# Performance work log

Hardware: AMD Instinct MI355X
Metric: run time of the kernel (lower is better)

## Reference

```python
import jax, jax.numpy as jnp
import numpy as np

L, H, D, BINS = 4, 8, 512, 16
HD = D // H
DFF = 4 * D
EPS = 1e-5


def _ln(x, g, b):
    mu = jnp.mean(x, axis=-1, keepdims=True)
    var = jnp.var(x, axis=-1, keepdims=True)
    return (x - mu) * jax.lax.rsqrt(var + EPS) * g + b


def setup_inputs() -> dict:
    key = jax.random.key(0)
    ks = jax.random.split(key, 24)
    B, N, F = 8, 1024, 4
    s = 0.02
    inp = {
        'slot_features': jax.random.normal(ks[0], (B, N, F), jnp.float32),
        'distance_matrix': jax.random.uniform(ks[1], (B, N, N), jnp.float32),
        'slot_mask': jnp.ones((B, N), dtype=bool),
        # input projection (Linear 4->D, then ReLU, then LayerNorm)
        'in_w': jax.random.normal(ks[2], (F, D), jnp.float32) * s,
        'in_b': jnp.zeros((D,), jnp.float32),
        'in_g': jnp.ones((D,), jnp.float32),
        'in_beta': jnp.zeros((D,), jnp.float32),
        # learnable distance bias, init linspace(0,-2) per head
        'dist_bias': jnp.tile(jnp.linspace(0.0, -2.0, BINS, dtype=jnp.float32)[None, :], (H, 1)),
        # per-layer stacked params (weights stored [in,out])
        'qkv_w': jax.random.normal(ks[3], (L, D, 3 * D), jnp.float32) * s,
        'qkv_b': jnp.zeros((L, 3 * D), jnp.float32),
        'out_w': jax.random.normal(ks[4], (L, D, D), jnp.float32) * s,
        'out_b': jnp.zeros((L, D), jnp.float32),
        'ffn_w1': jax.random.normal(ks[5], (L, D, DFF), jnp.float32) * s,
        'ffn_b1': jnp.zeros((L, DFF), jnp.float32),
        'ffn_w2': jax.random.normal(ks[6], (L, DFF, D), jnp.float32) * s,
        'ffn_b2': jnp.zeros((L, D), jnp.float32),
        'n1_g': jnp.ones((L, D), jnp.float32),
        'n1_b': jnp.zeros((L, D), jnp.float32),
        'n2_g': jnp.ones((L, D), jnp.float32),
        'n2_b': jnp.zeros((L, D), jnp.float32),
        'op_w': jax.random.normal(ks[7], (D, D), jnp.float32) * s,
        'op_b': jnp.zeros((D,), jnp.float32),
    }
    return inp


def _distance_bias(distance_matrix, slot_mask, dist_bias):
    # (B,H,N,N) additive attention bias from binned normalized distances
    max_dist = jnp.clip(jnp.max(distance_matrix, axis=(-1, -2), keepdims=True), 1e-6, None)
    norm_dist = distance_matrix / max_dist
    bin_idx = jnp.clip((norm_dist * (BINS - 1)).astype(jnp.int32), 0, BINS - 1)  # (B,N,N)
    bias = jnp.transpose(dist_bias.T[bin_idx], (0, 3, 1, 2))  # (B,N,N,H)->(B,H,N,N)
    pad = ~(slot_mask[:, :, None] & slot_mask[:, None, :])  # (B,N,N)
    return jnp.where(pad[:, None, :, :], -jnp.inf, bias)


def reference(slot_features, distance_matrix, slot_mask, in_w, in_b, in_g, in_beta,
              dist_bias, qkv_w, qkv_b, out_w, out_b, ffn_w1, ffn_b1, ffn_w2, ffn_b2,
              n1_g, n1_b, n2_g, n2_b, op_w, op_b):
    B, N, _ = slot_features.shape
    h = _ln(jax.nn.relu(slot_features @ in_w + in_b), in_g, in_beta)  # (B,N,D)
    attn_bias = _distance_bias(distance_matrix, slot_mask, dist_bias)  # (B,H,N,N)
    scale = 1.0 / jnp.sqrt(jnp.float32(HD))
    for i in range(L):
        hn = _ln(h, n1_g[i], n1_b[i])
        qkv = (hn @ qkv_w[i] + qkv_b[i]).reshape(B, N, 3, H, HD)
        q, k, v = (jnp.transpose(qkv[:, :, j], (0, 2, 1, 3)) for j in range(3))  # (B,H,N,HD)
        scores = jnp.einsum('bhnd,bhmd->bhnm', q, k) * scale + attn_bias
        attn = jax.nn.softmax(scores, axis=-1)
        o = jnp.einsum('bhnm,bhmd->bhnd', attn, v)
        o = jnp.transpose(o, (0, 2, 1, 3)).reshape(B, N, D)
        h = h + (o @ out_w[i] + out_b[i])
        hn2 = _ln(h, n2_g[i], n2_b[i])
        ff = jax.nn.gelu(hn2 @ ffn_w1[i] + ffn_b1[i], approximate=False) @ ffn_w2[i] + ffn_b2[i]
        h = h + ff
    return h @ op_w + op_b
```

## Files before the change

kernel.cpp:

```cpp
#include <hip/hip_runtime.h>


typedef __attribute__((ext_vector_type(8))) short short8;
typedef __attribute__((ext_vector_type(4))) float f32x4;

__device__ __forceinline__ float b2f(unsigned short u){
  return __uint_as_float(((unsigned)u) << 16);
}
__device__ __forceinline__ unsigned short f2b(float f){
  unsigned u = __float_as_uint(f);
  u += 0x7fffU + ((u >> 16) & 1U);
  return (unsigned short)(u >> 16);
}
__device__ __forceinline__ void gload16(const void* g, void* l){
  __builtin_amdgcn_global_load_lds((const __attribute__((address_space(1))) void*)g,
                                   (__attribute__((address_space(3))) void*)l, 16, 0, 0);
}

__global__ void transpose_w(const float* __restrict__ src, unsigned short* __restrict__ dst,
                            int K, int N){
  __shared__ float tile[32][33];
  const float* s = src + (size_t)blockIdx.z * K * N;
  unsigned short* d = dst + (size_t)blockIdx.z * K * N;
  int j = threadIdx.x & 31, i0 = threadIdx.x >> 5;
  int kt = blockIdx.y * 32, nt = blockIdx.x * 32;
#pragma unroll
  for (int s4 = 0; s4 < 4; ++s4){
    int i = i0 + s4 * 8;
    tile[i][j] = s[(size_t)(kt + i) * N + nt + j];
  }
  __syncthreads();
#pragma unroll
  for (int s4 = 0; s4 < 4; ++s4){
    int i = i0 + s4 * 8;
    d[(size_t)(nt + i) * K + kt + j] = f2b(tile[j][i]);
  }
}

__global__ void vt_kernel(const unsigned short* __restrict__ qkv, unsigned short* __restrict__ vt){
  __shared__ unsigned short tile[32][33];
  int tt = blockIdx.x, dt = blockIdx.y, bh = blockIdx.z;
  int b = bh >> 3, h = bh & 7;
  int j = threadIdx.x & 31, i0 = threadIdx.x >> 5;
#pragma unroll
  for (int s4 = 0; s4 < 4; ++s4){
    int i = i0 + s4 * 8;
    tile[i][j] = qkv[(size_t)(b * 1024 + tt * 32 + i) * 1536 + 1024 + h * 64 + dt * 32 + j];
  }
  __syncthreads();
#pragma unroll
  for (int s4 = 0; s4 < 4; ++s4){
    int i = i0 + s4 * 8;
    vt[(size_t)(bh * 64 + dt * 32 + i) * 1024 + tt * 32 + j] = tile[j][i];
  }
}

__global__ void bmax_kernel(const float* __restrict__ dist, unsigned* __restrict__ bmax){
  int b = blockIdx.x >> 5, sl = blockIdx.x & 31;
  const float* p = dist + (size_t)b * 1048576 + sl * 32768;
  int t = threadIdx.x;
  float m = 0.f;
  for (int i = t * 4; i < 32768; i += 1024){
    float4 v = *(const float4*)(p + i);
    m = fmaxf(m, fmaxf(fmaxf(v.x, v.y), fmaxf(v.z, v.w)));
  }
#pragma unroll
  for (int o = 1; o < 64; o <<= 1) m = fmaxf(m, __shfl_xor(m, o));
  __shared__ float wm[4];
  if ((t & 63) == 0) wm[t >> 6] = m;
  __syncthreads();
  if (t == 0){
    m = fmaxf(fmaxf(wm[0], wm[1]), fmaxf(wm[2], wm[3]));
    atomicMax(bmax + b, __float_as_uint(m));
  }
}

__global__ void bins_kernel(const float* __restrict__ dist, const unsigned* __restrict__ bmax,
                            unsigned char* __restrict__ out){
  int flat = blockIdx.x * 256 + threadIdx.x;
  int l15 = flat & 15, kt = (flat >> 4) & 15, q = (flat >> 8) & 1023, b = flat >> 18;
  float mx = fmaxf(__uint_as_float(bmax[b]), 1e-6f);
  const float* p = dist + ((size_t)(b * 1024 + q)) * 1024 + kt * 64 + l15;
  unsigned wd = 0;
#pragma unroll
  for (int ks = 0; ks < 4; ++ks){
    float v = p[ks * 16];
    int bi = (int)((v / mx) * 15.0f); bi = bi < 0 ? 0 : (bi > 15 ? 15 : bi);
    wd |= (unsigned)bi << (ks * 8);
  }
  *(unsigned*)(out + ((size_t)(b * 1024 + q)) * 1024 + kt * 64 + l15 * 4) = wd;
}

__global__ void inproj_kernel(const float* __restrict__ x, const float* __restrict__ w,
                              const float* __restrict__ b, const float* __restrict__ g,
                              const float* __restrict__ be, float* __restrict__ h){
  int t = threadIdx.x, wv = t >> 6, lane = t & 63;
  int row = blockIdx.x * 4 + wv;
  float x0 = x[row * 4 + 0], x1 = x[row * 4 + 1], x2 = x[row * 4 + 2], x3 = x[row * 4 + 3];
  int c0 = lane * 4, c1 = 256 + lane * 4;
  float4 v0, v1; float s = 0.f, sq = 0.f;
  {
    float4 w0 = *(const float4*)(w + c0), w1 = *(const float4*)(w + 512 + c0);
    float4 w2 = *(const float4*)(w + 1024 + c0), w3 = *(const float4*)(w + 1536 + c0);
    float4 bb = *(const float4*)(b + c0);
    v0.x = fmaxf(0.f, x0*w0.x + x1*w1.x + x2*w2.x + x3*w3.x + bb.x);
    v0.y = fmaxf(0.f, x0*w0.y + x1*w1.y + x2*w2.y + x3*w3.y + bb.y);
    v0.z = fmaxf(0.f, x0*w0.z + x1*w1.z + x2*w2.z + x3*w3.z + bb.z);
    v0.w = fmaxf(0.f, x0*w0.w + x1*w1.w + x2*w2.w + x3*w3.w + bb.w);
    s += v0.x + v0.y + v0.z + v0.w;
    sq += v0.x*v0.x + v0.y*v0.y + v0.z*v0.z + v0.w*v0.w;
  }
  {
    float4 w0 = *(const float4*)(w + c1), w1 = *(const float4*)(w + 512 + c1);
    float4 w2 = *(const float4*)(w + 1024 + c1), w3 = *(const float4*)(w + 1536 + c1);
    float4 bb = *(const float4*)(b + c1);
    v1.x = fmaxf(0.f, x0*w0.x + x1*w1.x + x2*w2.x + x3*w3.x + bb.x);
    v1.y = fmaxf(0.f, x0*w0.y + x1*w1.y + x2*w2.y + x3*w3.y + bb.y);
    v1.z = fmaxf(0.f, x0*w0.z + x1*w1.z + x2*w2.z + x3*w3.z + bb.z);
    v1.w = fmaxf(0.f, x0*w0.w + x1*w1.w + x2*w2.w + x3*w3.w + bb.w);
    s += v1.x + v1.y + v1.z + v1.w;
    sq += v1.x*v1.x + v1.y*v1.y + v1.z*v1.z + v1.w*v1.w;
  }
#pragma unroll
  for (int o = 1; o < 64; o <<= 1){ s += __shfl_xor(s, o); sq += __shfl_xor(sq, o); }
  float mu = s * (1.f / 512.f);
  float var = sq * (1.f / 512.f) - mu * mu;
  float rs = rsqrtf(var + 1e-5f);
  float* hp = h + (size_t)row * 512;
  {
    float4 gg = *(const float4*)(g + c0), bb = *(const float4*)(be + c0);
    float4 o4;
    o4.x = (v0.x - mu) * rs * gg.x + bb.x; o4.y = (v0.y - mu) * rs * gg.y + bb.y;
    o4.z = (v0.z - mu) * rs * gg.z + bb.z; o4.w = (v0.w - mu) * rs * gg.w + bb.w;
    *(float4*)(hp + c0) = o4;
  }
  {
    float4 gg = *(const float4*)(g + c1), bb = *(const float4*)(be + c1);
    float4 o4;
    o4.x = (v1.x - mu) * rs * gg.x + bb.x; o4.y = (v1.y - mu) * rs * gg.y + bb.y;
    o4.z = (v1.z - mu) * rs * gg.z + bb.z; o4.w = (v1.w - mu) * rs * gg.w + bb.w;
    *(float4*)(hp + c1) = o4;
  }
}

__global__ void ln_kernel(const float* __restrict__ h, const float* __restrict__ g,
                          const float* __restrict__ b, unsigned short* __restrict__ out){
  int t = threadIdx.x, wv = t >> 6, lane = t & 63;
  int row = blockIdx.x * 4 + wv;
  const float* hp = h + (size_t)row * 512;
  int c0 = lane * 4, c1 = 256 + lane * 4;
  float4 u0 = *(const float4*)(hp + c0);
  float4 u1 = *(const float4*)(hp + c1);
  float s = u0.x + u0.y + u0.z + u0.w + u1.x + u1.y + u1.z + u1.w;
  float sq = u0.x*u0.x + u0.y*u0.y + u0.z*u0.z + u0.w*u0.w
           + u1.x*u1.x + u1.y*u1.y + u1.z*u1.z + u1.w*u1.w;
#pragma unroll
  for (int o = 1; o < 64; o <<= 1){ s += __shfl_xor(s, o); sq += __shfl_xor(sq, o); }
  float mu = s * (1.f / 512.f);
  float var = sq * (1.f / 512.f) - mu * mu;
  float rs = rsqrtf(var + 1e-5f);
  unsigned short* op = out + (size_t)row * 512;
  {
    float4 gg = *(const float4*)(g + c0), bb = *(const float4*)(b + c0);
    ushort4 o4;
    o4.x = f2b((u0.x - mu) * rs * gg.x + bb.x); o4.y = f2b((u0.y - mu) * rs * gg.y + bb.y);
    o4.z = f2b((u0.z - mu) * rs * gg.z + bb.z); o4.w = f2b((u0.w - mu) * rs * gg.w + bb.w);
    *(ushort4*)(op + c0) = o4;
  }
  {
    float4 gg = *(const float4*)(g + c1), bb = *(const float4*)(b + c1);
    ushort4 o4;
    o4.x = f2b((u1.x - mu) * rs * gg.x + bb.x); o4.y = f2b((u1.y - mu) * rs * gg.y + bb.y);
    o4.z = f2b((u1.z - mu) * rs * gg.z + bb.z); o4.w = f2b((u1.w - mu) * rs * gg.w + bb.w);
    *(ushort4*)(op + c1) = o4;
  }
}

#define EPI_BF 0
#define EPI_RESID 1
#define EPI_GELU 2
#define EPI_RESID_BF 3
#define EPI_F32 4

template<int N, int K, int EPI>
__global__ __launch_bounds__(256) void gemm_k(
    const unsigned short* __restrict__ A,
    const unsigned short* __restrict__ Bt,
    const float* __restrict__ bias,
    float* __restrict__ resid,
    unsigned short* __restrict__ outb,
    float* __restrict__ outf)
{
  __shared__ unsigned short As[4096], Bs[4096];
  int t = threadIdx.x, w = t >> 6, lane = t & 63;
  int l15 = lane & 15, g = lane >> 4;
  int bm = blockIdx.x, bn = blockIdx.y;
  int wm = w >> 1, wn = w & 1;
  f32x4 acc[4][4];
#pragma unroll
  for (int i = 0; i < 4; ++i)
#pragma unroll
    for (int j = 0; j < 4; ++j) acc[i][j] = (f32x4){0.f, 0.f, 0.f, 0.f};

  for (int kt = 0; kt < K / 32; ++kt){
#pragma unroll
    for (int it = 0; it < 2; ++it){
      int ci = it * 4 + w;
      int o = ci * 1024 + lane * 16;
      int row = o >> 6, sp = (o >> 4) & 3;
      int sl = sp ^ ((row >> 1) & 3);
      gload16(A + (size_t)(bm * 128 + row) * K + kt * 32 + sl * 8, As + ci * 512);
      gload16(Bt + (size_t)(bn * 128 + row) * K + kt * 32 + sl * 8, Bs + ci * 512);
    }
    __syncthreads();
    short8 af[4], bf[4];
#pragma unroll
    for (int i = 0; i < 4; ++i){
      int row = wm * 64 + i * 16 + l15;
      int sp = g ^ ((row >> 1) & 3);
      af[i] = *(const short8*)(As + row * 32 + sp * 8);
    }
#pragma unroll
    for (int j = 0; j < 4; ++j){
      int row = wn * 64 + j * 16 + l15;
      int sp = g ^ ((row >> 1) & 3);
      bf[j] = *(const short8*)(Bs + row * 32 + sp * 8);
    }
#pragma unroll
    for (int i = 0; i < 4; ++i)
#pragma unroll
      for (int j = 0; j < 4; ++j)
        acc[i][j] = __builtin_amdgcn_mfma_f32_16x16x32_bf16(af[i], bf[j], acc[i][j], 0, 0, 0);
    __syncthreads();
  }
  int rbase = bm * 128 + wm * 64, cbase = bn * 128 + wn * 64;
#pragma unroll
  for (int j = 0; j < 4; ++j){
    int col = cbase + j * 16 + l15;
    float bs = bias[col];
#pragma unroll
    for (int i = 0; i < 4; ++i){
#pragma unroll
      for (int r = 0; r < 4; ++r){
        int row = rbase + i * 16 + g * 4 + r;
        size_t idx = (size_t)row * N + col;
        float x = acc[i][j][r] + bs;
        if constexpr (EPI == EPI_BF){
          outb[idx] = f2b(x);
        } else if constexpr (EPI == EPI_RESID){
          resid[idx] = resid[idx] + x;
        } else if constexpr (EPI == EPI_GELU){
          float y = 0.5f * x * (1.f + erff(x * 0.70710678118654752f));
          outb[idx] = f2b(y);
        } else if constexpr (EPI == EPI_RESID_BF){
          float y = resid[idx] + x;
          resid[idx] = y;
          outb[idx] = f2b(y);
        } else {
          outf[idx] = x;
        }
      }
    }
  }
}

__global__ __launch_bounds__(256) void attn_kernel(
    const unsigned short* __restrict__ qkv,
    const unsigned short* __restrict__ vt,
    const unsigned char* __restrict__ bins,
    const float* __restrict__ dist_bias,
    unsigned short* __restrict__ o_out)
{
  __shared__ unsigned short Ks[2][64 * 64];
  __shared__ unsigned short Vs[2][64 * 64];
  __shared__ unsigned short Ps[4][16 * 64];
  int bhx = blockIdx.x, qt = blockIdx.y;
  int b = bhx & 7, h = bhx >> 3;
  int bh = b * 8 + h;
  int t = threadIdx.x, w = t >> 6, lane = t & 63;
  int l15 = lane & 15, g = lane >> 4, rx = lane & 7;
  unsigned short* Psw = Ps[w];
  float lutv = dist_bias[h * 16 + l15];

  int qrow_frag = qt * 64 + w * 16 + l15;
  const unsigned short* qp = qkv + ((size_t)(b * 1024 + qrow_frag)) * 1536 + h * 64;
  short8 qf[2];
#pragma unroll
  for (int c = 0; c < 2; ++c){
    short8 raw = *(const short8*)(qp + c * 32 + g * 8);
#pragma unroll
    for (int e = 0; e < 8; ++e)
      raw[e] = (short)f2b(b2f((unsigned short)raw[e]) * 0.125f);
    qf[c] = raw;
  }

  float m_run[4], l_run[4];
  f32x4 acc_o[4];
#pragma unroll
  for (int r = 0; r < 4; ++r){ m_run[r] = -1e30f; l_run[r] = 0.f; }
#pragma unroll
  for (int d = 0; d < 4; ++d) acc_o[d] = (f32x4){0.f, 0.f, 0.f, 0.f};

  int qrow_c = qt * 64 + w * 16 + g * 4;
  int srow_lo = lane >> 3;
  int sslot = lane & 7;

  auto STAGE = [&](int buf, int kt){
#pragma unroll
    for (int it = 0; it < 2; ++it){
      int ci = it * 4 + w;
      int row = ci * 8 + srow_lo;
      int sl = sslot ^ (row & 7);
      gload16(qkv + (size_t)(b * 1024 + kt * 64 + row) * 1536 + 512 + h * 64 + sl * 8,
              &Ks[buf][ci * 512]);
      gload16(vt + (size_t)(bh * 64 + row) * 1024 + kt * 64 + sl * 8,
              &Vs[buf][ci * 512]);
    }
  };

  STAGE(0, 0);
  __syncthreads();
  int cur = 0;

  for (int kt = 0; kt < 16; ++kt){
    if (kt < 15) STAGE(cur ^ 1, kt + 1);

    const unsigned short* Kc = Ks[cur];
    const unsigned short* Vc = Vs[cur];

    f32x4 sv[4];
#pragma unroll
    for (int ks = 0; ks < 4; ++ks){
      f32x4 a = (f32x4){0.f, 0.f, 0.f, 0.f};
#pragma unroll
      for (int c = 0; c < 2; ++c){
        short8 kf = *(const short8*)(Kc + (ks * 16 + l15) * 64 + ((c * 4 + g) ^ rx) * 8);
        a = __builtin_amdgcn_mfma_f32_16x16x32_bf16(qf[c], kf, a, 0, 0, 0);
      }
      sv[ks] = a;
    }
    unsigned bw[4];
#pragma unroll
    for (int r = 0; r < 4; ++r)
      bw[r] = *(const unsigned*)(bins + (size_t)(b * 1024 + qrow_c + r) * 1024 + kt * 64 + l15 * 4);
#pragma unroll
    for (int r = 0; r < 4; ++r)
#pragma unroll
      for (int ks = 0; ks < 4; ++ks){
        int bin = (bw[r] >> (ks * 8)) & 255;
        sv[ks][r] += __shfl(lutv, bin);
      }
    float mt[4];
#pragma unroll
    for (int r = 0; r < 4; ++r)
      mt[r] = fmaxf(fmaxf(sv[0][r], sv[1][r]), fmaxf(sv[2][r], sv[3][r]));
#pragma unroll
    for (int o = 1; o < 16; o <<= 1)
#pragma unroll
      for (int r = 0; r < 4; ++r) mt[r] = fmaxf(mt[r], __shfl_xor(mt[r], o));
    float mnew[4], alpha[4];
#pragma unroll
    for (int r = 0; r < 4; ++r){
      mnew[r] = fmaxf(m_run[r], mt[r]);
      alpha[r] = __expf(m_run[r] - mnew[r]);
      m_run[r] = mnew[r];
    }
    float rs_[4] = {0.f, 0.f, 0.f, 0.f};
#pragma unroll
    for (int ks = 0; ks < 4; ++ks)
#pragma unroll
      for (int r = 0; r < 4; ++r){
        float p = __expf(sv[ks][r] - mnew[r]);
        rs_[r] += p;
        int prow = g * 4 + r;
        Psw[prow * 64 + ((ks * 2 + (l15 >> 3)) ^ (prow & 7)) * 8 + (l15 & 7)] = f2b(p);
      }
#pragma unroll
    for (int o = 1; o < 16; o <<= 1)
#pragma unroll
      for (int r = 0; r < 4; ++r) rs_[r] += __shfl_xor(rs_[r], o);
#pragma unroll
    for (int r = 0; r < 4; ++r) l_run[r] = l_run[r] * alpha[r] + rs_[r];
#pragma unroll
    for (int d = 0; d < 4; ++d){
      f32x4 ao = acc_o[d];
#pragma unroll
      for (int r = 0; r < 4; ++r) ao[r] *= alpha[r];
      acc_o[d] = ao;
    }
#pragma unroll
    for (int c = 0; c < 2; ++c){
      short8 pa = *(const short8*)(Psw + l15 * 64 + ((c * 4 + g) ^ rx) * 8);
#pragma unroll
      for (int d = 0; d < 4; ++d){
        short8 vf = *(const short8*)(Vc + (d * 16 + l15) * 64 + ((c * 4 + g) ^ rx) * 8);
        acc_o[d] = __builtin_amdgcn_mfma_f32_16x16x32_bf16(pa, vf, acc_o[d], 0, 0, 0);
      }
    }
    __syncthreads();
    cur ^= 1;
  }
#pragma unroll
  for (int d = 0; d < 4; ++d)
#pragma unroll
    for (int r = 0; r < 4; ++r){
      float v = acc_o[d][r] / l_run[r];
      size_t row = (size_t)(b * 1024 + qrow_c + r);
      o_out[row * 512 + h * 64 + d * 16 + l15] = f2b(v);
    }
}

extern "C" void kernel_launch(void* const* d_in, const int* in_sizes, int n_in,
                              void* d_out, int out_size, void* d_ws, size_t ws_size,
                              hipStream_t stream) {
  const float* x     = (const float*)d_in[0];
  const float* dist  = (const float*)d_in[1];
  const float* in_w  = (const float*)d_in[3];
  const float* in_b  = (const float*)d_in[4];
  const float* in_g  = (const float*)d_in[5];
  const float* in_be = (const float*)d_in[6];
  const float* dbias = (const float*)d_in[7];
  const float* qkv_w = (const float*)d_in[8];
  const float* qkv_b = (const float*)d_in[9];
  const float* out_w = (const float*)d_in[10];
  const float* out_b = (const float*)d_in[11];
  const float* f1_w  = (const float*)d_in[12];
  const float* f1_b  = (const float*)d_in[13];
  const float* f2_w  = (const float*)d_in[14];
  const float* f2_b  = (const float*)d_in[15];
  const float* n1g   = (const float*)d_in[16];
  const float* n1b   = (const float*)d_in[17];
  const float* n2g   = (const float*)d_in[18];
  const float* n2b   = (const float*)d_in[19];
  const float* op_w  = (const float*)d_in[20];
  const float* op_b  = (const float*)d_in[21];

  char* ws = (char*)d_ws;
  size_t off = 0;
  auto alloc = [&](size_t bytes){ size_t o = off; off += (bytes + 255) & ~(size_t)255; return o; };
  unsigned short* wqkv  = (unsigned short*)(ws + alloc((size_t)4 * 1536 * 512 * 2));
  unsigned short* wout  = (unsigned short*)(ws + alloc((size_t)4 * 512 * 512 * 2));
  unsigned short* wf1   = (unsigned short*)(ws + alloc((size_t)4 * 2048 * 512 * 2));
  unsigned short* wf2   = (unsigned short*)(ws + alloc((size_t)4 * 512 * 2048 * 2));
  unsigned short* wop   = (unsigned short*)(ws + alloc((size_t)512 * 512 * 2));
  float*          h     = (float*)(ws + alloc((size_t)8192 * 512 * 4));
  unsigned short* actbf = (unsigned short*)(ws + alloc((size_t)8192 * 512 * 2));
  unsigned short* qkvff = (unsigned short*)(ws + alloc((size_t)8192 * 2048 * 2));
  unsigned char*  binsb = (unsigned char*)(ws + alloc((size_t)8 * 1024 * 1024));
  unsigned*       bmax  = (unsigned*)(ws + alloc(256));
  unsigned short* vt    = qkvff + (size_t)8192 * 1536;
  (void)ws_size; (void)in_sizes; (void)n_in; (void)out_size;

  hipMemsetAsync(bmax, 0, 32, stream);
  transpose_w<<<dim3(48, 16, 4), 256, 0, stream>>>(qkv_w, wqkv, 512, 1536);
  transpose_w<<<dim3(16, 16, 4), 256, 0, stream>>>(out_w, wout, 512, 512);
  transpose_w<<<dim3(64, 16, 4), 256, 0, stream>>>(f1_w, wf1, 512, 2048);
  transpose_w<<<dim3(16, 64, 4), 256, 0, stream>>>(f2_w, wf2, 2048, 512);
  transpose_w<<<dim3(16, 16, 1), 256, 0, stream>>>(op_w, wop, 512, 512);
  bmax_kernel<<<256, 256, 0, stream>>>(dist, bmax);
  bins_kernel<<<8192, 256, 0, stream>>>(dist, bmax, binsb);
  inproj_kernel<<<2048, 256, 0, stream>>>(x, in_w, in_b, in_g, in_be, h);

  for (int l = 0; l < 4; ++l){
    ln_kernel<<<2048, 256, 0, stream>>>(h, n1g + l * 512, n1b + l * 512, actbf);
    gemm_k<1536, 512, EPI_BF><<<dim3(64, 12), 256, 0, stream>>>(
        actbf, wqkv + (size_t)l * 1536 * 512, qkv_b + l * 1536, nullptr, qkvff, nullptr);
    vt_kernel<<<dim3(32, 2, 64), 256, 0, stream>>>(qkvff, vt);
    attn_kernel<<<dim3(64, 16), 256, 0, stream>>>(qkvff, vt, binsb, dbias, actbf);
    gemm_k<512, 512, EPI_RESID><<<dim3(64, 4), 256, 0, stream>>>(
        actbf, wout + (size_t)l * 512 * 512, out_b + l * 512, h, nullptr, nullptr);
    ln_kernel<<<2048, 256, 0, stream>>>(h, n2g + l * 512, n2b + l * 512, actbf);
    gemm_k<2048, 512, EPI_GELU><<<dim3(64, 16), 256, 0, stream>>>(
        actbf, wf1 + (size_t)l * 2048 * 512, f1_b + l * 2048, nullptr, qkvff, nullptr);
    gemm_k<512, 2048, EPI_RESID_BF><<<dim3(64, 4), 256, 0, stream>>>(
        qkvff, wf2 + (size_t)l * 512 * 2048, f2_b + l * 512, h, actbf, nullptr);
  }
  gemm_k<512, 512, EPI_F32><<<dim3(64, 4), 256, 0, stream>>>(
      actbf, wop, op_b, nullptr, nullptr, (float*)d_out);
}
```

Baseline: 1.126 ms.

## Single-buffer K/V in attention, compute row sums via MFMA, add setprio

The attention kernel drops K/V double buffering in favour of a single LDS buffer loaded synchronously each tile, which halves LDS use so more blocks can be resident per CU. The softmax row-sum shuffle reduction is replaced by an extra MFMA of the bf16 P tile against a ones vector, and s_setprio brackets the MFMA sections. The trade is that global-load latency is no longer hidden inside a block, and the row sum now comes from bf16-rounded P, which slightly changes the normalisation.

```diff
diff --git a/kernel.cpp b/kernel.cpp
--- a/kernel.cpp
+++ b/kernel.cpp
@@ -271,8 +271,8 @@
     const float* __restrict__ dist_bias,
     unsigned short* __restrict__ o_out)
 {
-  __shared__ unsigned short Ks[2][64 * 64];
-  __shared__ unsigned short Vs[2][64 * 64];
+  __shared__ unsigned short Ks[64 * 64];
+  __shared__ unsigned short Vs[64 * 64];
   __shared__ unsigned short Ps[4][16 * 64];
   int bhx = blockIdx.x, qt = blockIdx.y;
   int b = bhx & 7, h = bhx >> 3;
@@ -294,51 +294,48 @@
     qf[c] = raw;
   }
 
-  float m_run[4], l_run[4];
-  f32x4 acc_o[4];
-#pragma unroll
-  for (int r = 0; r < 4; ++r){ m_run[r] = -1e30f; l_run[r] = 0.f; }
+  const short ONE = (short)0x3F80;
+  short8 ones = {ONE, ONE, ONE, ONE, ONE, ONE, ONE, ONE};
+
+  float m_run[4];
+  f32x4 acc_o[4], acc_s;
+#pragma unroll
+  for (int r = 0; r < 4; ++r) m_run[r] = -1e30f;
 #pragma unroll
   for (int d = 0; d < 4; ++d) acc_o[d] = (f32x4){0.f, 0.f, 0.f, 0.f};
+  acc_s = (f32x4){0.f, 0.f, 0.f, 0.f};
 
   int qrow_c = qt * 64 + w * 16 + g * 4;
   int srow_lo = lane >> 3;
   int sslot = lane & 7;
 
-  auto STAGE = [&](int buf, int kt){
+  for (int kt = 0; kt < 16; ++kt){
+    __syncthreads();
 #pragma unroll
     for (int it = 0; it < 2; ++it){
       int ci = it * 4 + w;
       int row = ci * 8 + srow_lo;
       int sl = sslot ^ (row & 7);
       gload16(qkv + (size_t)(b * 1024 + kt * 64 + row) * 1536 + 512 + h * 64 + sl * 8,
-              &Ks[buf][ci * 512]);
+              Ks + ci * 512);
       gload16(vt + (size_t)(bh * 64 + row) * 1024 + kt * 64 + sl * 8,
-              &Vs[buf][ci * 512]);
-    }
-  };
-
-  STAGE(0, 0);
-  __syncthreads();
-  int cur = 0;
-
-  for (int kt = 0; kt < 16; ++kt){
-    if (kt < 15) STAGE(cur ^ 1, kt + 1);
-
-    const unsigned short* Kc = Ks[cur];
-    const unsigned short* Vc = Vs[cur];
+              Vs + ci * 512);
+    }
+    __syncthreads();
 
     f32x4 sv[4];
+    __builtin_amdgcn_s_setprio(1);
 #pragma unroll
     for (int ks = 0; ks < 4; ++ks){
       f32x4 a = (f32x4){0.f, 0.f, 0.f, 0.f};
 #pragma unroll
       for (int c = 0; c < 2; ++c){
-        short8 kf = *(const short8*)(Kc + (ks * 16 + l15) * 64 + ((c * 4 + g) ^ rx) * 8);
+        short8 kf = *(const short8*)(Ks + (ks * 16 + l15) * 64 + ((c * 4 + g) ^ rx) * 8);
         a = __builtin_amdgcn_mfma_f32_16x16x32_bf16(qf[c], kf, a, 0, 0, 0);
       }
       sv[ks] = a;
     }
+    __builtin_amdgcn_s_setprio(0);
     unsigned bw[4];
 #pragma unroll
     for (int r = 0; r < 4; ++r)
@@ -358,30 +355,22 @@
     for (int o = 1; o < 16; o <<= 1)
 #pragma unroll
       for (int r = 0; r < 4; ++r) mt[r] = fmaxf(mt[r], __shfl_xor(mt[r], o));
-    float mnew[4], alpha[4];
+    float alpha[4];
 #pragma unroll
     for (int r = 0; r < 4; ++r){
-      mnew[r] = fmaxf(m_run[r], mt[r]);
-      alpha[r] = __expf(m_run[r] - mnew[r]);
-      m_run[r] = mnew[r];
-    }
-    float rs_[4] = {0.f, 0.f, 0.f, 0.f};
+      float mnew = fmaxf(m_run[r], mt[r]);
+      alpha[r] = __expf(m_run[r] - mnew);
+      m_run[r] = mnew;
+    }
 #pragma unroll
     for (int ks = 0; ks < 4; ++ks)
 #pragma unroll
       for (int r = 0; r < 4; ++r){
-        float p = __expf(sv[ks][r] - mnew[r]);
-        rs_[r] += p;
+        float p = __expf(sv[ks][r] - m_run[r]);
         int prow = g * 4 + r;
         Psw[prow * 64 + ((ks * 2 + (l15 >> 3)) ^ (prow & 7)) * 8 + (l15 & 7)] = f2b(p);
       }
 #pragma unroll
-    for (int o = 1; o < 16; o <<= 1)
-#pragma unroll
-      for (int r = 0; r < 4; ++r) rs_[r] += __shfl_xor(rs_[r], o);
-#pragma unroll
-    for (int r = 0; r < 4; ++r) l_run[r] = l_run[r] * alpha[r] + rs_[r];
-#pragma unroll
     for (int d = 0; d < 4; ++d){
       f32x4 ao = acc_o[d];
 #pragma unroll
@@ -389,22 +378,25 @@
       acc_o[d] = ao;
     }
 #pragma unroll
+    for (int r = 0; r < 4; ++r) acc_s[r] *= alpha[r];
+    __builtin_amdgcn_s_setprio(1);
+#pragma unroll
     for (int c = 0; c < 2; ++c){
       short8 pa = *(const short8*)(Psw + l15 * 64 + ((c * 4 + g) ^ rx) * 8);
+      acc_s = __builtin_amdgcn_mfma_f32_16x16x32_bf16(pa, ones, acc_s, 0, 0, 0);
 #pragma unroll
       for (int d = 0; d < 4; ++d){
-        short8 vf = *(const short8*)(Vc + (d * 16 + l15) * 64 + ((c * 4 + g) ^ rx) * 8);
+        short8 vf = *(const short8*)(Vs + (d * 16 + l15) * 64 + ((c * 4 + g) ^ rx) * 8);
         acc_o[d] = __builtin_amdgcn_mfma_f32_16x16x32_bf16(pa, vf, acc_o[d], 0, 0, 0);
       }
     }
-    __syncthreads();
-    cur ^= 1;
+    __builtin_amdgcn_s_setprio(0);
   }
 #pragma unroll
   for (int d = 0; d < 4; ++d)
 #pragma unroll
     for (int r = 0; r < 4; ++r){
-      float v = acc_o[d][r] / l_run[r];
+      float v = acc_o[d][r] / acc_s[r];
       size_t row = (size_t)(b * 1024 + qrow_c + r);
       o_out[row * 512 + h * 64 + d * 16 + l15] = f2b(v);
     }
```

Measured after the change: 1.015 ms. 1.11x faster.
